# Optimization experiments

Measured on AMD Instinct MI355X. Metric: run time of the kernel, lower is better.

## Reference

```python
import jax, jax.numpy as jnp
import numpy as np

VOCAB = 100000
DIM = 300
B = 65536
K = 10


def setup_inputs() -> dict:
    key = jax.random.key(0)
    k1, k2, k3, k4 = jax.random.split(key, 4)
    initrange = 1.0 / DIM
    u_weight = jax.random.uniform(k1, (VOCAB, DIM), jnp.float32, -initrange, initrange)
    v_weight = jnp.zeros((VOCAB, DIM), jnp.float32)
    pos_u = jax.random.randint(k2, (B,), 0, VOCAB)
    pos_v = jax.random.randint(k3, (B,), 0, VOCAB)
    neg_v = jax.random.randint(k4, (B, K), 0, VOCAB)
    return {"u_weight": u_weight, "v_weight": v_weight,
            "pos_u": pos_u, "pos_v": pos_v, "neg_v": neg_v}


def reference(u_weight, v_weight, pos_u, pos_v, neg_v):
    emb_u = u_weight[pos_u]          # [B, D]
    emb_v = v_weight[pos_v]          # [B, D]
    emb_neg_v = v_weight[neg_v]      # [B, K, D]

    score = jnp.sum(emb_u * emb_v, axis=1)               # [B]
    score = jnp.clip(score, -10.0, 10.0)
    pos_loss = -jax.nn.log_sigmoid(score)                # [B]

    neg_score = jnp.einsum('bkd,bd->bk', emb_neg_v, emb_u)  # [B, K]
    neg_score = jnp.clip(neg_score, -10.0, 10.0)
    neg_loss = -jnp.sum(jax.nn.log_sigmoid(-neg_score), axis=1)  # [B]

    return jnp.mean(pos_loss + neg_loss)
```

## Files before the change

kernel.cpp:

```cpp
#include <hip/hip_runtime.h>
#include <math.h>


#define DIM   300
#define B_TOT 65536
#define K_NEG 10
#define NROW  (K_NEG + 2)

constexpr int BLOCKS = 4096;
constexpr int TPB    = 256;
constexpr int WAVES  = BLOCKS * (TPB / 64);
constexpr int B_PER_WAVE = B_TOT / WAVES;

typedef float vf4 __attribute__((ext_vector_type(4)));

__device__ __forceinline__ float dot4(vf4 a, vf4 b) {
    vf4 p = a * b;
    return p.x + p.y + p.z + p.w;
}

__device__ __forceinline__ vf4 ld_nt(const vf4* p) {
    return __builtin_nontemporal_load(p);
}

__global__ __launch_bounds__(TPB, 4) void sg_main(
    const float* __restrict__ uw, const float* __restrict__ vw,
    const int* __restrict__ pos_u, const int* __restrict__ pos_v,
    const int* __restrict__ neg_v, float* __restrict__ block_sums)
{
    const int lane = threadIdx.x & 63;
    const int wib  = threadIdx.x >> 6;
    int gw = blockIdx.x * (TPB / 64) + wib;
    gw = __builtin_amdgcn_readfirstlane(gw);

    const bool c1ok = lane < (75 - 64);
    const int  o2   = c1ok ? (64 + lane) : lane;

    float acc = 0.f;

    #pragma unroll 1
    for (int i = 0; i < B_PER_WAVE; ++i) {
        const int b = gw * B_PER_WAVE + i;

        const int iu = pos_u[b];
        const int iv = pos_v[b];
        int nx[K_NEG];
        #pragma unroll
        for (int k = 0; k < K_NEG; ++k) nx[k] = neg_v[b * K_NEG + k];

        const vf4* pr[NROW];
        pr[0] = (const vf4*)(uw + (size_t)iu * DIM);
        pr[1] = (const vf4*)(vw + (size_t)iv * DIM);
        #pragma unroll
        for (int k = 0; k < K_NEG; ++k)
            pr[2 + k] = (const vf4*)(vw + (size_t)nx[k] * DIM);

        vf4 c0[NROW];
        vf4 c1[NROW];
        c0[0] = ld_nt(pr[0] + lane);
        c1[0] = ld_nt(pr[0] + o2);
        #pragma unroll
        for (int j = 1; j < NROW; ++j) c0[j] = pr[j][lane];
        #pragma unroll
        for (int j = 1; j < NROW; ++j) c1[j] = pr[j][o2];

        float part[K_NEG + 1];
        #pragma unroll
        for (int j = 1; j < NROW; ++j) {
            float p = dot4(c0[j], c0[0]);
            float q = dot4(c1[j], c1[0]);
            part[j - 1] = p + (c1ok ? q : 0.f);
        }

        #pragma unroll
        for (int s = 1; s < 64; s <<= 1) {
            #pragma unroll
            for (int j = 0; j < K_NEG + 1; ++j)
                part[j] += __shfl_xor(part[j], s, 64);
        }

        float score = fminf(fmaxf(part[0], -10.f), 10.f);
        float loss = __logf(1.f + __expf(-score));
        #pragma unroll
        for (int k = 0; k < K_NEG; ++k) {
            float ns = fminf(fmaxf(part[k + 1], -10.f), 10.f);
            loss += __logf(1.f + __expf(ns));
        }
        acc += loss;
    }

    __shared__ float red[TPB / 64];
    if (lane == 0) red[wib] = acc;
    __syncthreads();
    if (threadIdx.x == 0)
        block_sums[blockIdx.x] = red[0] + red[1] + red[2] + red[3];
}

__global__ __launch_bounds__(256) void sg_finalize(
    const float* __restrict__ bs, float* __restrict__ out)
{
    float s = 0.f;
    for (int i = threadIdx.x; i < BLOCKS; i += 256) s += bs[i];
    #pragma unroll
    for (int off = 1; off < 64; off <<= 1) s += __shfl_xor(s, off, 64);
    __shared__ float red[4];
    const int wave = threadIdx.x >> 6;
    if ((threadIdx.x & 63) == 0) red[wave] = s;
    __syncthreads();
    if (threadIdx.x == 0)
        out[0] = (red[0] + red[1] + red[2] + red[3]) * (1.0f / (float)B_TOT);
}

extern "C" void kernel_launch(void* const* d_in, const int* in_sizes, int n_in,
                              void* d_out, int out_size, void* d_ws, size_t ws_size,
                              hipStream_t stream) {
    const float* uw    = (const float*)d_in[0];
    const float* vw    = (const float*)d_in[1];
    const int*   pos_u = (const int*)d_in[2];
    const int*   pos_v = (const int*)d_in[3];
    const int*   neg_v = (const int*)d_in[4];
    float* out = (float*)d_out;
    float* block_sums = (float*)d_ws;

    sg_main<<<BLOCKS, TPB, 0, stream>>>(uw, vw, pos_u, pos_v, neg_v, block_sums);
    sg_finalize<<<1, 256, 0, stream>>>(block_sums, out);
}
```

Measured before the change: 335.1 us.

## Prefetch next sample's rows before reduction and preload all indices

```diff
diff --git a/kernel.cpp b/kernel.cpp
--- a/kernel.cpp
+++ b/kernel.cpp
@@ -36,41 +36,54 @@
     const bool c1ok = lane < (75 - 64);
     const int  o2   = c1ok ? (64 + lane) : lane;
 
+    const int b0 = gw * B_PER_WAVE;
+
+    int idx[B_PER_WAVE][NROW];
+    #pragma unroll
+    for (int i = 0; i < B_PER_WAVE; ++i) {
+        idx[i][0] = __builtin_amdgcn_readfirstlane(pos_u[b0 + i]);
+        idx[i][1] = __builtin_amdgcn_readfirstlane(pos_v[b0 + i]);
+        #pragma unroll
+        for (int k = 0; k < K_NEG; ++k)
+            idx[i][2 + k] = __builtin_amdgcn_readfirstlane(neg_v[(b0 + i) * K_NEG + k]);
+    }
+
+    vf4 c0[NROW];
+    vf4 c1[NROW];
+
+    auto issue = [&](int i) {
+        {
+            const vf4* bu = (const vf4*)(uw + (size_t)idx[i][0] * DIM);
+            c0[0] = ld_nt(bu + lane);
+            c1[0] = ld_nt(bu + o2);
+        }
+        #pragma unroll
+        for (int j = 1; j < NROW; ++j) {
+            const vf4* bv = (const vf4*)(vw + (size_t)idx[i][j] * DIM);
+            c0[j] = bv[lane];
+            c1[j] = bv[o2];
+        }
+    };
+
+    issue(0);
+
     float acc = 0.f;
 
-    #pragma unroll 1
+    #pragma unroll
     for (int i = 0; i < B_PER_WAVE; ++i) {
-        const int b = gw * B_PER_WAVE + i;
-
-        const int iu = pos_u[b];
-        const int iv = pos_v[b];
-        int nx[K_NEG];
-        #pragma unroll
-        for (int k = 0; k < K_NEG; ++k) nx[k] = neg_v[b * K_NEG + k];
-
-        const vf4* pr[NROW];
-        pr[0] = (const vf4*)(uw + (size_t)iu * DIM);
-        pr[1] = (const vf4*)(vw + (size_t)iv * DIM);
-        #pragma unroll
-        for (int k = 0; k < K_NEG; ++k)
-            pr[2 + k] = (const vf4*)(vw + (size_t)nx[k] * DIM);
-
-        vf4 c0[NROW];
-        vf4 c1[NROW];
-        c0[0] = ld_nt(pr[0] + lane);
-        c1[0] = ld_nt(pr[0] + o2);
-        #pragma unroll
-        for (int j = 1; j < NROW; ++j) c0[j] = pr[j][lane];
-        #pragma unroll
-        for (int j = 1; j < NROW; ++j) c1[j] = pr[j][o2];
+        const vf4 u0 = c0[0];
+        const vf4 u1 = c1[0];
 
         float part[K_NEG + 1];
         #pragma unroll
         for (int j = 1; j < NROW; ++j) {
-            float p = dot4(c0[j], c0[0]);
-            float q = dot4(c1[j], c1[0]);
+            float p = dot4(c0[j], u0);
+            float q = dot4(c1[j], u1);
             part[j - 1] = p + (c1ok ? q : 0.f);
         }
+
+        if (i + 1 < B_PER_WAVE) issue(i + 1);
+        __builtin_amdgcn_sched_barrier(0x7);
 
         #pragma unroll
         for (int s = 1; s < 64; s <<= 1) {
```

Result: slower. 349.3 us (+4.2%).
